# Kernel tuning notes

Hardware: AMD Instinct MI355X
Metric: run time of the kernel (lower is better)

## Reference

```python
import jax, jax.numpy as jnp
import numpy as np

NUM_NODES = 100000
E = 512    # embedding_size
U = 64     # embedding_u_size
T = 8      # edge_type_count
A = 32     # dim_a
B = 8192   # batch
NB = 10    # neighbors per type


def setup_inputs() -> dict:
    key = jax.random.key(0)
    ks = jax.random.split(key, 8)
    std = 1.0 / np.sqrt(E)
    return {
        "node_embeddings": jax.random.uniform(ks[0], (NUM_NODES, E), jnp.float32, -1.0, 1.0),
        "node_type_embeddings": jax.random.uniform(ks[1], (NUM_NODES, T, U), jnp.float32, -1.0, 1.0),
        "trans_weights": jax.random.normal(ks[2], (T, U, E), jnp.float32) * std,
        "trans_weights_s1": jax.random.normal(ks[3], (T, U, A), jnp.float32) * std,
        "trans_weights_s2": jax.random.normal(ks[4], (T, A, 1), jnp.float32) * std,
        "train_inputs": jax.random.randint(ks[5], (B,), 0, NUM_NODES, jnp.int32),
        "train_types": jax.random.randint(ks[6], (B,), 0, T, jnp.int32),
        "node_neigh": jax.random.randint(ks[7], (B, T, NB), 0, NUM_NODES, jnp.int32),
    }


def reference(node_embeddings, node_type_embeddings, trans_weights,
              trans_weights_s1, trans_weights_s2,
              train_inputs, train_types, node_neigh):
    # node_embed: [B, E]
    node_embed = node_embeddings[train_inputs]
    # Per-type neighbor gather. Original materializes [B,T,NB,T,U] then takes the
    # diagonal over the two type axes; we gather only the diagonal directly:
    # neigh_embed[b,t,n,:] = node_type_embeddings[node_neigh[b,t,n], t, :]
    type_idx = jnp.arange(T)[None, :, None]              # [1,T,1]
    neigh_embed = node_type_embeddings[node_neigh, type_idx]  # [B,T,NB,U]
    node_type_embed = neigh_embed.sum(axis=2)            # [B,T,U]

    # Per-sample gathered projection weights (MoE-style by edge type)
    w_s1 = trans_weights_s1[train_types]                 # [B,U,A]
    w_s2 = trans_weights_s2[train_types]                 # [B,A,1]
    w = trans_weights[train_types]                       # [B,U,E]

    # attention over edge types
    h = jnp.tanh(jnp.einsum('btu,bua->bta', node_type_embed, w_s1))  # [B,T,A]
    scores = jnp.einsum('bta,bao->bt', h, w_s2)          # [B,T] (squeeze of [B,T,1])
    attention = jax.nn.softmax(scores, axis=-1)          # [B,T]

    agg = jnp.einsum('bt,btu->bu', attention, node_type_embed)  # [B,U]
    node_embed = node_embed + jnp.einsum('bu,bue->be', agg, w)  # [B,E]

    # F.normalize(dim=1): divide by L2 norm clamped at 1e-12
    norm = jnp.maximum(jnp.linalg.norm(node_embed, axis=1, keepdims=True), 1e-12)
    return node_embed / norm
```

## Files before the change

### kernel.cpp

```cpp
#include <hip/hip_runtime.h>

#define E_DIM 512
#define U_DIM 64
#define T_DIM 8
#define A_DIM 32
#define NB    10
#define BATCH 8192

__launch_bounds__(256, 4)
__global__ void gatne_kernel(
    const float* __restrict__ node_embeddings,
    const float* __restrict__ node_type_embeddings,
    const float* __restrict__ trans_weights,
    const float* __restrict__ trans_weights_s1,
    const float* __restrict__ trans_weights_s2,
    const int*   __restrict__ train_inputs,
    const int*   __restrict__ train_types,
    const int*   __restrict__ node_neigh,
    float*       __restrict__ out)
{
    const int b   = blockIdx.x;
    const int tid = threadIdx.x;

    __shared__ int   s_neigh[T_DIM * NB];
    __shared__ float s_nte[T_DIM][U_DIM];
    __shared__ float s_w1[U_DIM * A_DIM];
    __shared__ float s_w2[A_DIM];
    __shared__ float s_att[T_DIM];
    __shared__ float s_agg[U_DIM];
    __shared__ float s_red[4];

    const int ni = train_inputs[b];
    const int ty = train_types[b];

    if (tid < T_DIM * NB) s_neigh[tid] = node_neigh[b * (T_DIM * NB) + tid];
    for (int i = tid; i < U_DIM * A_DIM; i += 256)
        s_w1[i] = trans_weights_s1[ty * (U_DIM * A_DIM) + i];
    if (tid < A_DIM) s_w2[tid] = trans_weights_s2[ty * A_DIM + tid];
    __syncthreads();

    {
        const int u = tid & 63;
        const int g = tid >> 6;
        #pragma unroll
        for (int k = 0; k < 2; ++k) {
            const int t = g + 4 * k;
            float acc = 0.f;
            #pragma unroll
            for (int n = 0; n < NB; ++n) {
                const int nb = s_neigh[t * NB + n];
                acc += node_type_embeddings[(size_t)nb * (T_DIM * U_DIM) + t * U_DIM + u];
            }
            s_nte[t][u] = acc;
        }
    }
    __syncthreads();

    {
        const int t = tid >> 5;
        const int a = tid & 31;
        float hsum = 0.f;
        #pragma unroll
        for (int u = 0; u < U_DIM; ++u)
            hsum += s_nte[t][u] * s_w1[u * A_DIM + a];
        float val = tanhf(hsum) * s_w2[a];
        #pragma unroll
        for (int off = 16; off > 0; off >>= 1)
            val += __shfl_down(val, off, 32);
        if (a == 0) s_att[t] = val;
    }
    __syncthreads();

    if (tid == 0) {
        float m = s_att[0];
        #pragma unroll
        for (int t = 1; t < T_DIM; ++t) m = fmaxf(m, s_att[t]);
        float e[T_DIM], sum = 0.f;
        #pragma unroll
        for (int t = 0; t < T_DIM; ++t) { e[t] = __expf(s_att[t] - m); sum += e[t]; }
        const float inv = 1.f / sum;
        #pragma unroll
        for (int t = 0; t < T_DIM; ++t) s_att[t] = e[t] * inv;
    }
    __syncthreads();

    if (tid < U_DIM) {
        float acc = 0.f;
        #pragma unroll
        for (int t = 0; t < T_DIM; ++t)
            acc += s_att[t] * s_nte[t][tid];
        s_agg[tid] = acc;
    }
    __syncthreads();

    const int e0 = tid * 2;
    const float2 ne = *(const float2*)(node_embeddings + (size_t)ni * E_DIM + e0);
    float v0 = ne.x, v1 = ne.y;
    const float* wbase = trans_weights + (size_t)ty * (U_DIM * E_DIM) + e0;
    #pragma unroll 8
    for (int u = 0; u < U_DIM; ++u) {
        const float a = s_agg[u];
        const float2 wv = *(const float2*)(wbase + (size_t)u * E_DIM);
        v0 = fmaf(a, wv.x, v0);
        v1 = fmaf(a, wv.y, v1);
    }

    float ss = v0 * v0 + v1 * v1;
    #pragma unroll
    for (int off = 32; off > 0; off >>= 1)
        ss += __shfl_down(ss, off, 64);
    if ((tid & 63) == 0) s_red[tid >> 6] = ss;
    __syncthreads();
    const float total = s_red[0] + s_red[1] + s_red[2] + s_red[3];
    const float inv = 1.f / fmaxf(sqrtf(total), 1e-12f);

    float2 o; o.x = v0 * inv; o.y = v1 * inv;
    *(float2*)(out + (size_t)b * E_DIM + e0) = o;
}

extern "C" void kernel_launch(void* const* d_in, const int* in_sizes, int n_in,
                              void* d_out, int out_size, void* d_ws, size_t ws_size,
                              hipStream_t stream) {
    const float* node_embeddings      = (const float*)d_in[0];
    const float* node_type_embeddings = (const float*)d_in[1];
    const float* trans_weights        = (const float*)d_in[2];
    const float* trans_weights_s1     = (const float*)d_in[3];
    const float* trans_weights_s2     = (const float*)d_in[4];
    const int*   train_inputs         = (const int*)d_in[5];
    const int*   train_types          = (const int*)d_in[6];
    const int*   node_neigh           = (const int*)d_in[7];
    float* out = (float*)d_out;

    gatne_kernel<<<BATCH, 256, 0, stream>>>(
        node_embeddings, node_type_embeddings, trans_weights,
        trans_weights_s1, trans_weights_s2,
        train_inputs, train_types, node_neigh, out);
}
```

Baseline: 415.5 us.

## Process one batch sample per wavefront with wave-level sync and shuffles

Each 64-lane wavefront now handles one batch sample, four samples per block, instead of one block per sample. Block-wide __syncthreads and the shared staging of the attention weights are replaced by wave barriers, register shuffles and direct global reads, and the softmax runs redundantly in every lane. Each lane issues the neighbor gather loads early and uses float4 loads and stores for the output projection. This is meant to cut synchronization overhead and raise per-thread memory-level parallelism, at the cost of more registers per thread and less parallelism within each sample.

```diff
diff --git a/kernel.cpp b/kernel.cpp
--- a/kernel.cpp
+++ b/kernel.cpp
@@ -6,6 +6,7 @@
 #define A_DIM 32
 #define NB    10
 #define BATCH 8192
+#define WPB   4
 
 __launch_bounds__(256, 4)
 __global__ void gatne_kernel(
@@ -19,103 +20,109 @@
     const int*   __restrict__ node_neigh,
     float*       __restrict__ out)
 {
-    const int b   = blockIdx.x;
-    const int tid = threadIdx.x;
+    const int tid  = threadIdx.x;
+    const int lane = tid & 63;
+    const int wv   = tid >> 6;
+    const int b    = blockIdx.x * WPB + wv;
 
-    __shared__ int   s_neigh[T_DIM * NB];
-    __shared__ float s_nte[T_DIM][U_DIM];
-    __shared__ float s_w1[U_DIM * A_DIM];
-    __shared__ float s_w2[A_DIM];
-    __shared__ float s_att[T_DIM];
-    __shared__ float s_agg[U_DIM];
-    __shared__ float s_red[4];
+    __shared__ float s_nte[WPB][T_DIM][U_DIM];
+    __shared__ float s_agg[WPB][U_DIM];
 
     const int ni = train_inputs[b];
     const int ty = train_types[b];
 
-    if (tid < T_DIM * NB) s_neigh[tid] = node_neigh[b * (T_DIM * NB) + tid];
-    for (int i = tid; i < U_DIM * A_DIM; i += 256)
-        s_w1[i] = trans_weights_s1[ty * (U_DIM * A_DIM) + i];
-    if (tid < A_DIM) s_w2[tid] = trans_weights_s2[ty * A_DIM + tid];
-    __syncthreads();
+    const float* neb = node_embeddings + (size_t)ni * E_DIM + lane * 8;
+    const float4 ne0 = *(const float4*)(neb);
+    const float4 ne1 = *(const float4*)(neb + 4);
 
-    {
-        const int u = tid & 63;
-        const int g = tid >> 6;
+    const int* nn = node_neigh + (size_t)b * (T_DIM * NB);
+    const int idx0 = nn[lane];
+    const int idx1 = (lane < (T_DIM * NB - 64)) ? nn[64 + lane] : 0;
+
+    float acc[T_DIM];
+    #pragma unroll
+    for (int t = 0; t < T_DIM; ++t) {
+        float a = 0.f;
         #pragma unroll
-        for (int k = 0; k < 2; ++k) {
-            const int t = g + 4 * k;
-            float acc = 0.f;
-            #pragma unroll
-            for (int n = 0; n < NB; ++n) {
-                const int nb = s_neigh[t * NB + n];
-                acc += node_type_embeddings[(size_t)nb * (T_DIM * U_DIM) + t * U_DIM + u];
-            }
-            s_nte[t][u] = acc;
+        for (int n = 0; n < NB; ++n) {
+            const int j = t * NB + n;
+            const int nbi = (j < 64) ? __shfl(idx0, j, 64)
+                                     : __shfl(idx1, j - 64, 64);
+            a += node_type_embeddings[(size_t)nbi * (T_DIM * U_DIM) + t * U_DIM + lane];
         }
+        acc[t] = a;
+        s_nte[wv][t][lane] = a;
     }
-    __syncthreads();
+    __builtin_amdgcn_wave_barrier();
 
-    {
-        const int t = tid >> 5;
-        const int a = tid & 31;
-        float hsum = 0.f;
-        #pragma unroll
-        for (int u = 0; u < U_DIM; ++u)
-            hsum += s_nte[t][u] * s_w1[u * A_DIM + a];
-        float val = tanhf(hsum) * s_w2[a];
-        #pragma unroll
-        for (int off = 16; off > 0; off >>= 1)
-            val += __shfl_down(val, off, 32);
-        if (a == 0) s_att[t] = val;
+    const int a_idx = lane & 31;
+    const int half  = lane >> 5;
+    const float* w1 = trans_weights_s1 + (size_t)ty * (U_DIM * A_DIM) + a_idx;
+    float h0 = 0.f, h1 = 0.f, h2 = 0.f, h3 = 0.f;
+    #pragma unroll
+    for (int u = 0; u < U_DIM; ++u) {
+        const float wv1 = w1[u * A_DIM];
+        h0 = fmaf(s_nte[wv][half + 0][u], wv1, h0);
+        h1 = fmaf(s_nte[wv][half + 2][u], wv1, h1);
+        h2 = fmaf(s_nte[wv][half + 4][u], wv1, h2);
+        h3 = fmaf(s_nte[wv][half + 6][u], wv1, h3);
     }
-    __syncthreads();
+    const float w2v = trans_weights_s2[ty * A_DIM + a_idx];
+    h0 = tanhf(h0) * w2v;
+    h1 = tanhf(h1) * w2v;
+    h2 = tanhf(h2) * w2v;
+    h3 = tanhf(h3) * w2v;
+    #pragma unroll
+    for (int off = 16; off > 0; off >>= 1) {
+        h0 += __shfl_down(h0, off, 32);
+        h1 += __shfl_down(h1, off, 32);
+        h2 += __shfl_down(h2, off, 32);
+        h3 += __shfl_down(h3, off, 32);
+    }
+    const float s0 = __shfl(h0, 0, 64),  s2 = __shfl(h1, 0, 64);
+    const float s4 = __shfl(h2, 0, 64),  s6 = __shfl(h3, 0, 64);
+    const float s1 = __shfl(h0, 32, 64), s3 = __shfl(h1, 32, 64);
+    const float s5 = __shfl(h2, 32, 64), s7 = __shfl(h3, 32, 64);
 
-    if (tid == 0) {
-        float m = s_att[0];
-        #pragma unroll
-        for (int t = 1; t < T_DIM; ++t) m = fmaxf(m, s_att[t]);
-        float e[T_DIM], sum = 0.f;
-        #pragma unroll
-        for (int t = 0; t < T_DIM; ++t) { e[t] = __expf(s_att[t] - m); sum += e[t]; }
-        const float inv = 1.f / sum;
-        #pragma unroll
-        for (int t = 0; t < T_DIM; ++t) s_att[t] = e[t] * inv;
-    }
-    __syncthreads();
+    const float m = fmaxf(fmaxf(fmaxf(s0, s1), fmaxf(s2, s3)),
+                          fmaxf(fmaxf(s4, s5), fmaxf(s6, s7)));
+    const float e0 = __expf(s0 - m), e1 = __expf(s1 - m);
+    const float e2 = __expf(s2 - m), e3 = __expf(s3 - m);
+    const float e4 = __expf(s4 - m), e5 = __expf(s5 - m);
+    const float e6 = __expf(s6 - m), e7 = __expf(s7 - m);
+    const float inv_sum = 1.f / (e0 + e1 + e2 + e3 + e4 + e5 + e6 + e7);
 
-    if (tid < U_DIM) {
-        float acc = 0.f;
-        #pragma unroll
-        for (int t = 0; t < T_DIM; ++t)
-            acc += s_att[t] * s_nte[t][tid];
-        s_agg[tid] = acc;
-    }
-    __syncthreads();
+    const float agg = (e0 * acc[0] + e1 * acc[1] + e2 * acc[2] + e3 * acc[3] +
+                       e4 * acc[4] + e5 * acc[5] + e6 * acc[6] + e7 * acc[7]) * inv_sum;
+    s_agg[wv][lane] = agg;
+    __builtin_amdgcn_wave_barrier();
 
-    const int e0 = tid * 2;
-    const float2 ne = *(const float2*)(node_embeddings + (size_t)ni * E_DIM + e0);
-    float v0 = ne.x, v1 = ne.y;
-    const float* wbase = trans_weights + (size_t)ty * (U_DIM * E_DIM) + e0;
+    const float* wb = trans_weights + (size_t)ty * (U_DIM * E_DIM) + lane * 8;
+    float4 v0 = ne0, v1 = ne1;
     #pragma unroll 8
     for (int u = 0; u < U_DIM; ++u) {
-        const float a = s_agg[u];
-        const float2 wv = *(const float2*)(wbase + (size_t)u * E_DIM);
-        v0 = fmaf(a, wv.x, v0);
-        v1 = fmaf(a, wv.y, v1);
+        const float av = s_agg[wv][u];
+        const float4 w0  = *(const float4*)(wb + (size_t)u * E_DIM);
+        const float4 w1v = *(const float4*)(wb + (size_t)u * E_DIM + 4);
+        v0.x = fmaf(av, w0.x, v0.x);  v0.y = fmaf(av, w0.y, v0.y);
+        v0.z = fmaf(av, w0.z, v0.z);  v0.w = fmaf(av, w0.w, v0.w);
+        v1.x = fmaf(av, w1v.x, v1.x); v1.y = fmaf(av, w1v.y, v1.y);
+        v1.z = fmaf(av, w1v.z, v1.z); v1.w = fmaf(av, w1v.w, v1.w);
     }
 
-    float ss = v0 * v0 + v1 * v1;
+    float ss = v0.x * v0.x + v0.y * v0.y + v0.z * v0.z + v0.w * v0.w
+             + v1.x * v1.x + v1.y * v1.y + v1.z * v1.z + v1.w * v1.w;
     #pragma unroll
     for (int off = 32; off > 0; off >>= 1)
-        ss += __shfl_down(ss, off, 64);
-    if ((tid & 63) == 0) s_red[tid >> 6] = ss;
-    __syncthreads();
-    const float total = s_red[0] + s_red[1] + s_red[2] + s_red[3];
-    const float inv = 1.f / fmaxf(sqrtf(total), 1e-12f);
+        ss += __shfl_xor(ss, off, 64);
+    const float inv = 1.f / fmaxf(sqrtf(ss), 1e-12f);
 
-    float2 o; o.x = v0 * inv; o.y = v1 * inv;
-    *(float2*)(out + (size_t)b * E_DIM + e0) = o;
+    float4 o0, o1;
+    o0.x = v0.x * inv; o0.y = v0.y * inv; o0.z = v0.z * inv; o0.w = v0.w * inv;
+    o1.x = v1.x * inv; o1.y = v1.y * inv; o1.z = v1.z * inv; o1.w = v1.w * inv;
+    float* ob = out + (size_t)b * E_DIM + lane * 8;
+    *(float4*)(ob)     = o0;
+    *(float4*)(ob + 4) = o1;
 }
 
 extern "C" void kernel_launch(void* const* d_in, const int* in_sizes, int n_in,
@@ -131,7 +138,7 @@
     const int*   node_neigh           = (const int*)d_in[7];
     float* out = (float*)d_out;
 
-    gatne_kernel<<<BATCH, 256, 0, stream>>>(
+    gatne_kernel<<<BATCH / WPB, 256, 0, stream>>>(
         node_embeddings, node_type_embeddings, trans_weights,
         trans_weights_s1, trans_weights_s2,
         train_inputs, train_types, node_neigh, out);
```

Result: slower. 517.8 us (+24.6%).

## Drop shared staging of weights and indices, fuse softmax with aggregation

Applied to the files above, without the earlier changes.

Removes the shared-memory copies of neighbor indices and the s1/s2 weight slices. Each wavefront now loads its own neighbor indices into registers and broadcasts them with shuffles, and the attention matvec reads s1 weights straight from global memory. The softmax is fused into the aggregation step, which removes one barrier, and the node embedding load is issued early so its latency overlaps the gather. Shared memory per block shrinks and launch bounds rise to 8 blocks per CU to raise occupancy, at the cost of tighter register limits and repeated global reads of the weights.

```diff
diff --git a/kernel.cpp b/kernel.cpp
--- a/kernel.cpp
+++ b/kernel.cpp
@@ -7,7 +7,7 @@
 #define NB    10
 #define BATCH 8192
 
-__launch_bounds__(256, 4)
+__launch_bounds__(256, 8)
 __global__ void gatne_kernel(
     const float* __restrict__ node_embeddings,
     const float* __restrict__ node_type_embeddings,
@@ -19,51 +19,47 @@
     const int*   __restrict__ node_neigh,
     float*       __restrict__ out)
 {
-    const int b   = blockIdx.x;
-    const int tid = threadIdx.x;
+    const int b    = blockIdx.x;
+    const int tid  = threadIdx.x;
+    const int lane = tid & 63;
+    const int wv   = tid >> 6;
 
-    __shared__ int   s_neigh[T_DIM * NB];
     __shared__ float s_nte[T_DIM][U_DIM];
-    __shared__ float s_w1[U_DIM * A_DIM];
-    __shared__ float s_w2[A_DIM];
     __shared__ float s_att[T_DIM];
     __shared__ float s_agg[U_DIM];
     __shared__ float s_red[4];
 
+    const int* nn = node_neigh + (size_t)b * (T_DIM * NB);
+    int my = 0;
+    if (lane < 2 * NB) my = nn[wv * NB + (lane < NB ? lane : 30 + lane)];
+
     const int ni = train_inputs[b];
     const int ty = train_types[b];
 
-    if (tid < T_DIM * NB) s_neigh[tid] = node_neigh[b * (T_DIM * NB) + tid];
-    for (int i = tid; i < U_DIM * A_DIM; i += 256)
-        s_w1[i] = trans_weights_s1[ty * (U_DIM * A_DIM) + i];
-    if (tid < A_DIM) s_w2[tid] = trans_weights_s2[ty * A_DIM + tid];
-    __syncthreads();
+    const int e0 = tid * 2;
+    const float2 ne = *(const float2*)(node_embeddings + (size_t)ni * E_DIM + e0);
 
-    {
-        const int u = tid & 63;
-        const int g = tid >> 6;
-        #pragma unroll
-        for (int k = 0; k < 2; ++k) {
-            const int t = g + 4 * k;
-            float acc = 0.f;
-            #pragma unroll
-            for (int n = 0; n < NB; ++n) {
-                const int nb = s_neigh[t * NB + n];
-                acc += node_type_embeddings[(size_t)nb * (T_DIM * U_DIM) + t * U_DIM + u];
-            }
-            s_nte[t][u] = acc;
-        }
+    float a0 = 0.f, a1 = 0.f;
+    #pragma unroll
+    for (int n = 0; n < NB; ++n) {
+        const int i0 = __shfl(my, n, 64);
+        const int i1 = __shfl(my, NB + n, 64);
+        a0 += node_type_embeddings[(size_t)i0 * (T_DIM * U_DIM) + wv * U_DIM + lane];
+        a1 += node_type_embeddings[(size_t)i1 * (T_DIM * U_DIM) + (wv + 4) * U_DIM + lane];
     }
+    s_nte[wv][lane]     = a0;
+    s_nte[wv + 4][lane] = a1;
     __syncthreads();
 
     {
         const int t = tid >> 5;
         const int a = tid & 31;
-        float hsum = 0.f;
+        const float* w1 = trans_weights_s1 + (size_t)ty * (U_DIM * A_DIM) + a;
+        float h = 0.f;
         #pragma unroll
         for (int u = 0; u < U_DIM; ++u)
-            hsum += s_nte[t][u] * s_w1[u * A_DIM + a];
-        float val = tanhf(hsum) * s_w2[a];
+            h = fmaf(s_nte[t][u], w1[u * A_DIM], h);
+        float val = tanhf(h) * trans_weights_s2[ty * A_DIM + a];
         #pragma unroll
         for (int off = 16; off > 0; off >>= 1)
             val += __shfl_down(val, off, 32);
@@ -71,45 +67,39 @@
     }
     __syncthreads();
 
-    if (tid == 0) {
-        float m = s_att[0];
-        #pragma unroll
-        for (int t = 1; t < T_DIM; ++t) m = fmaxf(m, s_att[t]);
-        float e[T_DIM], sum = 0.f;
-        #pragma unroll
-        for (int t = 0; t < T_DIM; ++t) { e[t] = __expf(s_att[t] - m); sum += e[t]; }
-        const float inv = 1.f / sum;
-        #pragma unroll
-        for (int t = 0; t < T_DIM; ++t) s_att[t] = e[t] * inv;
+    if (tid < U_DIM) {
+        float sc0 = s_att[0], sc1 = s_att[1], sc2 = s_att[2], sc3 = s_att[3];
+        float sc4 = s_att[4], sc5 = s_att[5], sc6 = s_att[6], sc7 = s_att[7];
+        const float m = fmaxf(fmaxf(fmaxf(sc0, sc1), fmaxf(sc2, sc3)),
+                              fmaxf(fmaxf(sc4, sc5), fmaxf(sc6, sc7)));
+        const float x0 = __expf(sc0 - m), x1 = __expf(sc1 - m);
+        const float x2 = __expf(sc2 - m), x3 = __expf(sc3 - m);
+        const float x4 = __expf(sc4 - m), x5 = __expf(sc5 - m);
+        const float x6 = __expf(sc6 - m), x7 = __expf(sc7 - m);
+        const float inv_sum = 1.f / (x0 + x1 + x2 + x3 + x4 + x5 + x6 + x7);
+        const float acc = x0 * s_nte[0][tid] + x1 * s_nte[1][tid]
+                        + x2 * s_nte[2][tid] + x3 * s_nte[3][tid]
+                        + x4 * s_nte[4][tid] + x5 * s_nte[5][tid]
+                        + x6 * s_nte[6][tid] + x7 * s_nte[7][tid];
+        s_agg[tid] = acc * inv_sum;
     }
     __syncthreads();
 
-    if (tid < U_DIM) {
-        float acc = 0.f;
-        #pragma unroll
-        for (int t = 0; t < T_DIM; ++t)
-            acc += s_att[t] * s_nte[t][tid];
-        s_agg[tid] = acc;
-    }
-    __syncthreads();
-
-    const int e0 = tid * 2;
-    const float2 ne = *(const float2*)(node_embeddings + (size_t)ni * E_DIM + e0);
+    const float* wb = trans_weights + (size_t)ty * (U_DIM * E_DIM) + e0;
     float v0 = ne.x, v1 = ne.y;
-    const float* wbase = trans_weights + (size_t)ty * (U_DIM * E_DIM) + e0;
-    #pragma unroll 8
+    #pragma unroll 16
     for (int u = 0; u < U_DIM; ++u) {
-        const float a = s_agg[u];
-        const float2 wv = *(const float2*)(wbase + (size_t)u * E_DIM);
-        v0 = fmaf(a, wv.x, v0);
-        v1 = fmaf(a, wv.y, v1);
+        const float av = s_agg[u];
+        const float2 w2v = *(const float2*)(wb + (size_t)u * E_DIM);
+        v0 = fmaf(av, w2v.x, v0);
+        v1 = fmaf(av, w2v.y, v1);
     }
 
     float ss = v0 * v0 + v1 * v1;
     #pragma unroll
     for (int off = 32; off > 0; off >>= 1)
-        ss += __shfl_down(ss, off, 64);
-    if ((tid & 63) == 0) s_red[tid >> 6] = ss;
+        ss += __shfl_xor(ss, off, 64);
+    if (lane == 0) s_red[wv] = ss;
     __syncthreads();
     const float total = s_red[0] + s_red[1] + s_red[2] + s_red[3];
     const float inv = 1.f / fmaxf(sqrtf(total), 1e-12f);
```

After: 416.7 us. About the same (+0.3%).
